# Optimization experiments

Hardware: AMD Instinct MI355X
Metric: run time of the kernel (lower is better)

## Reference

```python
import jax, jax.numpy as jnp
import numpy as np


def setup_inputs() -> dict:
    key = jax.random.key(0)
    k1, k2, k3, k4 = jax.random.split(key, 4)
    N, M, D = 4096, 4096, 1024
    H = jax.random.normal(k1, (N, D), dtype=jnp.float32)
    K = jax.random.normal(k2, (M, D), dtype=jnp.float32)
    V = jax.random.normal(k3, (M, D), dtype=jnp.float32)
    attn_mask = jax.random.uniform(k4, (N, M), dtype=jnp.float32)
    return {"H": H, "K": K, "V": V, "attn_mask": attn_mask}


def reference(H, K, V, attn_mask):
    # scores: [N, M] = H @ K^T, scaled by sqrt(d)
    d = H.shape[1]
    scores = jnp.matmul(H, K.T) / jnp.sqrt(jnp.asarray(d, dtype=H.dtype))
    # double softmax with elementwise mask multiply in between
    probs = jax.nn.softmax(jax.nn.softmax(scores, axis=1) * attn_mask, axis=1)
    return jnp.matmul(probs, V)
```

## Files before the change

### kernel.cpp

```cpp
#include <hip/hip_runtime.h>
#include <cstdint>

typedef unsigned short u16;
typedef __bf16 bf16x8 __attribute__((ext_vector_type(8)));
typedef float f32x4 __attribute__((ext_vector_type(4)));
typedef unsigned int u32x4 __attribute__((ext_vector_type(4)));

__device__ __forceinline__ float bf2f(u16 h) {
  union { unsigned int u; float f; } v; v.u = ((unsigned int)h) << 16; return v.f;
}
__device__ __forceinline__ u16 f2bf(float f) {
  union { float f; unsigned int u; } v; v.f = f;
  unsigned int u = v.u;
  return (u16)((u + 0x7FFFu + ((u >> 16) & 1u)) >> 16);
}

__device__ __forceinline__ void ld_lds16(const void* g, void* l) {
  __builtin_amdgcn_global_load_lds(
      (const __attribute__((address_space(1))) unsigned int*)g,
      (__attribute__((address_space(3))) unsigned int*)l, 16, 0, 0);
}

__global__ __launch_bounds__(512, 2) void gemm1_kernel(
    const u16* __restrict__ A, const u16* __restrict__ B,
    u16* __restrict__ S, int ldA, int ldB, int ldC)
{
  __shared__ __align__(16) u16 smem[65536];

  const int tid  = threadIdx.x;
  const int lane = tid & 63;
  const int w    = tid >> 6;
  const int wr   = w >> 2;
  const int wc   = w & 3;
  const int quad = lane >> 4;
  const int cIn  = lane & 15;
  const int lrow   = lane >> 3;
  const int gchunk = (lane & 7) ^ lrow;

  const int flat = blockIdx.x;
  const int xcd  = flat & 7;
  const int i    = flat >> 3;
  const int rowT = (xcd >> 1) * 4 + (i & 3);
  const int colT = (xcd & 1) * 8 + (i >> 2);
  const int rowBlk = rowT * 256;
  const int colBlk = colT * 256;

  f32x4 acc[8][4];
  #pragma unroll
  for (int a = 0; a < 8; ++a)
    #pragma unroll
    for (int b = 0; b < 4; ++b) acc[a][b] = {0.f, 0.f, 0.f, 0.f};

  auto stageA = [&](int buf, int kt2) {
    #pragma unroll
    for (int l = 0; l < 4; ++l) {
      const u16* ga = A + (size_t)(rowBlk + l * 64 + w * 8 + lrow) * ldA
                        + kt2 * 64 + gchunk * 8;
      ld_lds16(ga, &smem[buf * 16384 + l * 4096 + w * 512]);
    }
  };
  auto stageB = [&](int buf, int kt2) {
    #pragma unroll
    for (int l = 0; l < 4; ++l) {
      const u16* gb = B + (size_t)(colBlk + l * 64 + w * 8 + lrow) * ldB
                        + kt2 * 64 + gchunk * 8;
      ld_lds16(gb, &smem[32768 + buf * 16384 + l * 4096 + w * 512]);
    }
  };

  stageA(0, 0);
  stageB(0, 0);
  stageA(1, 1);
  stageB(1, 1);

  for (int kt = 0; kt < 16; ++kt) {
    const int cur = kt & 1;
    const int aBase = cur * 16384;
    const int bBase = 32768 + cur * 16384;

    if (kt < 15) asm volatile("s_waitcnt vmcnt(8)" ::: "memory");
    else         asm volatile("s_waitcnt vmcnt(0)" ::: "memory");
    __builtin_amdgcn_s_barrier();
    __builtin_amdgcn_sched_barrier(0);

    bf16x8 bf[4][2];
    #pragma unroll
    for (int ni = 0; ni < 4; ++ni)
      #pragma unroll
      for (int ks = 0; ks < 2; ++ks) {
        int row = wc * 64 + ni * 16 + cIn;
        int ch  = (ks * 4 + quad) ^ (row & 7);
        bf[ni][ks] = *(const bf16x8*)&smem[bBase + row * 64 + ch * 8];
      }
    bf16x8 afA[2][2], afB[2][2];
    #pragma unroll
    for (int m = 0; m < 2; ++m)
      #pragma unroll
      for (int ks = 0; ks < 2; ++ks) {
        int row = wr * 128 + m * 16 + cIn;
        int ch  = (ks * 4 + quad) ^ (row & 7);
        afA[m][ks] = *(const bf16x8*)&smem[aBase + row * 64 + ch * 8];
      }

    #pragma unroll
    for (int q = 0; q < 4; ++q) {
      if (q < 3) {
        #pragma unroll
        for (int m = 0; m < 2; ++m)
          #pragma unroll
          for (int ks = 0; ks < 2; ++ks) {
            int row = wr * 128 + ((q + 1) * 2 + m) * 16 + cIn;
            int ch  = (ks * 4 + quad) ^ (row & 7);
            bf16x8 v = *(const bf16x8*)&smem[aBase + row * 64 + ch * 8];
            if (q & 1) afA[m][ks] = v; else afB[m][ks] = v;
          }
      }
      __builtin_amdgcn_sched_barrier(0);
      __builtin_amdgcn_s_barrier();
      __builtin_amdgcn_sched_barrier(0);
      __builtin_amdgcn_s_setprio(1);
      #pragma unroll
      for (int m = 0; m < 2; ++m)
        #pragma unroll
        for (int ni = 0; ni < 4; ++ni)
          #pragma unroll
          for (int ks = 0; ks < 2; ++ks) {
            if (q & 1)
              acc[q * 2 + m][ni] = __builtin_amdgcn_mfma_f32_16x16x32_bf16(
                  afB[m][ks], bf[ni][ks], acc[q * 2 + m][ni], 0, 0, 0);
            else
              acc[q * 2 + m][ni] = __builtin_amdgcn_mfma_f32_16x16x32_bf16(
                  afA[m][ks], bf[ni][ks], acc[q * 2 + m][ni], 0, 0, 0);
          }
      __builtin_amdgcn_s_setprio(0);
      __builtin_amdgcn_sched_barrier(0);
    }
    __builtin_amdgcn_s_barrier();

    if (kt + 2 < 16) {
      stageA(cur, kt + 2);
      stageB(cur, kt + 2);
    }
  }

  const float scale = 0.03125f;
  u16* epi = smem;
  #pragma unroll
  for (int R = 0; R < 2; ++R) {
    #pragma unroll
    for (int m2 = 0; m2 < 4; ++m2) {
      int mi = R * 4 + m2;
      #pragma unroll
      for (int ni = 0; ni < 4; ++ni) {
        int col = wc * 64 + ni * 16 + cIn;
        #pragma unroll
        for (int r = 0; r < 4; ++r) {
          int er = wr * 64 + m2 * 16 + quad * 4 + r;
          epi[er * 264 + col] = f2bf(acc[mi][ni][r] * scale);
        }
      }
    }
    __syncthreads();
    #pragma unroll
    for (int it = 0; it < 8; ++it) {
      int idx = it * 512 + tid;
      int er  = idx >> 5;
      int c8  = idx & 31;
      int grow = rowBlk + (er >> 6) * 128 + R * 64 + (er & 63);
      u32x4 v = *(const u32x4*)&epi[er * 264 + c8 * 8];
      *(u32x4*)&S[(size_t)grow * ldC + colBlk + c8 * 8] = v;
    }
    __syncthreads();
  }
}

__global__ __launch_bounds__(512, 2) void gemm2_kernel(
    const u16* __restrict__ A, const u16* __restrict__ B,
    float* __restrict__ Out, const float* __restrict__ L2,
    int ldA, int ldB, int ldC)
{
  __shared__ __align__(16) u16 smem[49152];

  const int tid  = threadIdx.x;
  const int lane = tid & 63;
  const int w    = tid >> 6;
  const int wk   = w & 1;
  const int wrow = (w >> 1) & 1;
  const int wcol = (w >> 2) & 1;
  const int quad = lane >> 4;
  const int cIn  = lane & 15;
  const int lrow   = lane >> 3;
  const int gchunk = (lane & 7) ^ lrow;

  const int flat = blockIdx.x;
  const int xcd  = flat & 7;
  const int i    = flat >> 3;
  const int rowBlk = (xcd * 4 + (i & 3)) * 128;
  const int colBlk = (i >> 2) * 128;

  f32x4 acc[4][4];
  #pragma unroll
  for (int a = 0; a < 4; ++a)
    #pragma unroll
    for (int b = 0; b < 4; ++b) acc[a][b] = {0.f, 0.f, 0.f, 0.f};

  auto stage = [&](int buf, int kt) {
    int kk = kt * 64;
    #pragma unroll
    for (int t = 0; t < 2; ++t) {
      int rg = w * 2 + t;
      const u16* ga = A + (size_t)(rowBlk + rg * 8 + lrow) * ldA + kk + gchunk * 8;
      ld_lds16(ga, &smem[buf * 8192 + rg * 512]);
      const u16* gb = B + (size_t)(colBlk + rg * 8 + lrow) * ldB + kk + gchunk * 8;
      ld_lds16(gb, &smem[24576 + buf * 8192 + rg * 512]);
    }
  };

  stage(0, 0);
  stage(1, 1);

  int cur = 0;
  for (int kt = 0; kt < 64; ++kt) {
    if (kt < 63) asm volatile("s_waitcnt vmcnt(4)" ::: "memory");
    else         asm volatile("s_waitcnt vmcnt(0)" ::: "memory");
    __builtin_amdgcn_s_barrier();
    __builtin_amdgcn_sched_barrier(0);

    if (kt + 2 < 64) {
      int nb = cur + 2; if (nb >= 3) nb -= 3;
      stage(nb, kt + 2);
    }

    const int aBase = cur * 8192;
    const int bBase = 24576 + cur * 8192;
    bf16x8 af[4], bfr[4];
    #pragma unroll
    for (int mi = 0; mi < 4; ++mi) {
      int row = wrow * 64 + mi * 16 + cIn;
      int ch  = (wk * 4 + quad) ^ (row & 7);
      af[mi]  = *(const bf16x8*)&smem[aBase + row * 64 + ch * 8];
    }
    #pragma unroll
    for (int ni = 0; ni < 4; ++ni) {
      int row = wcol * 64 + ni * 16 + cIn;
      int ch  = (wk * 4 + quad) ^ (row & 7);
      bfr[ni] = *(const bf16x8*)&smem[bBase + row * 64 + ch * 8];
    }
    __builtin_amdgcn_s_setprio(1);
    #pragma unroll
    for (int mi = 0; mi < 4; ++mi)
      #pragma unroll
      for (int ni = 0; ni < 4; ++ni)
        acc[mi][ni] = __builtin_amdgcn_mfma_f32_16x16x32_bf16(
            af[mi], bfr[ni], acc[mi][ni], 0, 0, 0);
    __builtin_amdgcn_s_setprio(0);

    cur = (cur + 1 == 3) ? 0 : cur + 1;
  }

  float* red = (float*)smem;
  const int ow = w >> 1;
  const int rbase = ow * 4160 + lane * 65;
  __syncthreads();
  if (wk == 1) {
    #pragma unroll
    for (int mi = 0; mi < 4; ++mi)
      #pragma unroll
      for (int ni = 0; ni < 4; ++ni)
        #pragma unroll
        for (int r = 0; r < 4; ++r)
          red[rbase + (mi * 4 + ni) * 4 + r] = acc[mi][ni][r];
  }
  __syncthreads();
  if (wk == 0) {
    #pragma unroll
    for (int mi = 0; mi < 4; ++mi) {
      #pragma unroll
      for (int r = 0; r < 4; ++r) {
        int row   = rowBlk + wrow * 64 + mi * 16 + quad * 4 + r;
        float inv = 1.0f / L2[row];
        #pragma unroll
        for (int ni = 0; ni < 4; ++ni) {
          int col = colBlk + wcol * 64 + ni * 16 + cIn;
          float v = acc[mi][ni][r] + red[rbase + (mi * 4 + ni) * 4 + r];
          __builtin_nontemporal_store(v * inv, &Out[(size_t)row * ldC + col]);
        }
      }
    }
  }
}

__global__ __launch_bounds__(256) void prep_kernel(
    const float* __restrict__ H, const float* __restrict__ Kin,
    const float* __restrict__ V, u16* __restrict__ Hb, u16* __restrict__ Kb,
    u16* __restrict__ Vt)
{
  int b = blockIdx.x;
  if (b < 8192) {
    const float* src = (b < 4096) ? H : Kin;
    u16* dst = (b < 4096) ? Hb : Kb;
    int i = (b & 4095) * 256 + threadIdx.x;
    f32x4 v = __builtin_nontemporal_load(&((const f32x4*)src)[i]);
    ushort4 o;
    o.x = f2bf(v.x); o.y = f2bf(v.y); o.z = f2bf(v.z); o.w = f2bf(v.w);
    ((ushort4*)dst)[i] = o;
  } else {
    __shared__ float tile[32][33];
    b -= 8192;
    int c0 = (b & 31) * 32;
    int r0 = (b >> 5) * 32;
    int tx = threadIdx.x & 31, ty = threadIdx.x >> 5;
    #pragma unroll
    for (int s = 0; s < 32; s += 8)
      tile[ty + s][tx] = __builtin_nontemporal_load(
          &V[(size_t)(r0 + ty + s) * 1024 + c0 + tx]);
    __syncthreads();
    if (threadIdx.x < 128) {
      int vr = threadIdx.x >> 2;
      int ch = threadIdx.x & 3;
      u32x4 ov;
      #pragma unroll
      for (int p = 0; p < 4; ++p) {
        unsigned int lo = f2bf(tile[ch * 8 + p * 2][vr]);
        unsigned int hi = f2bf(tile[ch * 8 + p * 2 + 1][vr]);
        ov[p] = lo | (hi << 16);
      }
      *(u32x4*)&Vt[(size_t)(c0 + vr) * 4096 + r0 + ch * 8] = ov;
    }
  }
}

__global__ __launch_bounds__(256) void softmax2_kernel(
    u16* __restrict__ S, const float* __restrict__ mask,
    float* __restrict__ L2, int M)
{
  int row = blockIdx.x;
  u16* srow = S + (size_t)row * M;
  const float* mrow = mask + (size_t)row * M;
  const int base = threadIdx.x * 16;

  u16 sl[16];
  *(uint4*)(sl)     = *(const uint4*)(srow + base);
  *(uint4*)(sl + 8) = *(const uint4*)(srow + base + 8);

  float e[16];
  float s1 = 0.f;
  #pragma unroll
  for (int j = 0; j < 16; ++j) { e[j] = __expf(bf2f(sl[j])); s1 += e[j]; }

  __shared__ float wred[8];
  #pragma unroll
  for (int m = 1; m < 64; m <<= 1) s1 += __shfl_xor(s1, m, 64);
  if ((threadIdx.x & 63) == 0) wred[threadIdx.x >> 6] = s1;
  __syncthreads();
  float inv = 1.0f / (wred[0] + wred[1] + wred[2] + wred[3]);

  float mv[16];
  #pragma unroll
  for (int q = 0; q < 4; ++q) {
    f32x4 m4 = __builtin_nontemporal_load((const f32x4*)(mrow + base + q * 4));
    mv[q * 4 + 0] = m4.x; mv[q * 4 + 1] = m4.y;
    mv[q * 4 + 2] = m4.z; mv[q * 4 + 3] = m4.w;
  }

  float lsum = 0.f;
  #pragma unroll
  for (int j = 0; j < 16; ++j) {
    float p = __expf(e[j] * inv * mv[j]);
    lsum += p;
    sl[j] = f2bf(p);
  }
  *(uint4*)(srow + base)     = *(uint4*)(sl);
  *(uint4*)(srow + base + 8) = *(uint4*)(sl + 8);

  #pragma unroll
  for (int m = 1; m < 64; m <<= 1) lsum += __shfl_xor(lsum, m, 64);
  if ((threadIdx.x & 63) == 0) wred[4 + (threadIdx.x >> 6)] = lsum;
  __syncthreads();
  if (threadIdx.x == 0) L2[row] = wred[4] + wred[5] + wred[6] + wred[7];
}

extern "C" void kernel_launch(void* const* d_in, const int* in_sizes, int n_in,
                              void* d_out, int out_size, void* d_ws, size_t ws_size,
                              hipStream_t stream) {
  const float* H    = (const float*)d_in[0];
  const float* Kin  = (const float*)d_in[1];
  const float* V    = (const float*)d_in[2];
  const float* mask = (const float*)d_in[3];
  float* out = (float*)d_out;

  const int N = 4096, M = 4096, D = 1024;

  char* ws = (char*)d_ws;
  u16*   Hb = (u16*)(ws);
  u16*   Kb = (u16*)(ws + (8ull << 20));
  u16*   Vt = (u16*)(ws + (16ull << 20));
  u16*   S  = (u16*)(ws + (24ull << 20));
  float* L2 = (float*)(ws + (56ull << 20));

  prep_kernel<<<dim3(12288), dim3(256), 0, stream>>>(H, Kin, V, Hb, Kb, Vt);

  gemm1_kernel<<<dim3(256), dim3(512), 0, stream>>>(Hb, Kb, S, D, D, M);

  softmax2_kernel<<<dim3(N), dim3(256), 0, stream>>>(S, mask, L2, M);

  gemm2_kernel<<<dim3(256), dim3(512), 0, stream>>>(S, Vt, out, L2, M, M, D);
}
```

Before: 228.1 us.

## Interleave A-tile global-to-LDS loads per quarter across MFMA phases in gemm1

Splits the A-tile staging into four quarter-sized loads and issues them between the four MFMA phases of each k-step, instead of issuing all A and B loads after the whole k-step finishes. The goal is to spread global-to-LDS traffic through the compute loop, overlap memory latency with MFMA work, and remove the trailing barrier before prefetch. In exchange it adds more barriers and finer vmcnt/lgkmcnt waits whose counts must exactly match outstanding loads, so a miscount could create a race or extra stalls.

```diff
diff --git a/kernel.cpp b/kernel.cpp
--- a/kernel.cpp
+++ b/kernel.cpp
@@ -51,14 +51,6 @@
     #pragma unroll
     for (int b = 0; b < 4; ++b) acc[a][b] = {0.f, 0.f, 0.f, 0.f};
 
-  auto stageA = [&](int buf, int kt2) {
-    #pragma unroll
-    for (int l = 0; l < 4; ++l) {
-      const u16* ga = A + (size_t)(rowBlk + l * 64 + w * 8 + lrow) * ldA
-                        + kt2 * 64 + gchunk * 8;
-      ld_lds16(ga, &smem[buf * 16384 + l * 4096 + w * 512]);
-    }
-  };
   auto stageB = [&](int buf, int kt2) {
     #pragma unroll
     for (int l = 0; l < 4; ++l) {
@@ -67,56 +59,48 @@
       ld_lds16(gb, &smem[32768 + buf * 16384 + l * 4096 + w * 512]);
     }
   };
-
-  stageA(0, 0);
+  auto stageAq = [&](int buf, int kt2, int q) {
+    int rbase = ((w & 4) << 5) + q * 32 + (w & 3) * 8;
+    const u16* ga = A + (size_t)(rowBlk + rbase + lrow) * ldA
+                      + kt2 * 64 + gchunk * 8;
+    ld_lds16(ga, &smem[buf * 16384 + rbase * 64]);
+  };
+
   stageB(0, 0);
-  stageA(1, 1);
+  stageAq(0, 0, 0); stageAq(0, 0, 1); stageAq(0, 0, 2); stageAq(0, 0, 3);
   stageB(1, 1);
+  stageAq(1, 1, 0); stageAq(1, 1, 1); stageAq(1, 1, 2);
+  asm volatile("s_waitcnt vmcnt(10)" ::: "memory");
+  __builtin_amdgcn_s_barrier();
 
   for (int kt = 0; kt < 16; ++kt) {
-    const int cur = kt & 1;
-    const int aBase = cur * 16384;
-    const int bBase = 32768 + cur * 16384;
-
-    if (kt < 15) asm volatile("s_waitcnt vmcnt(8)" ::: "memory");
-    else         asm volatile("s_waitcnt vmcnt(0)" ::: "memory");
-    __builtin_amdgcn_s_barrier();
-    __builtin_amdgcn_sched_barrier(0);
+    const int c = kt & 1;
+    const int aBase = c * 16384;
+    const int bBase = 32768 + c * 16384;
 
     bf16x8 bf[4][2];
-    #pragma unroll
-    for (int ni = 0; ni < 4; ++ni)
-      #pragma unroll
-      for (int ks = 0; ks < 2; ++ks) {
-        int row = wc * 64 + ni * 16 + cIn;
-        int ch  = (ks * 4 + quad) ^ (row & 7);
-        bf[ni][ks] = *(const bf16x8*)&smem[bBase + row * 64 + ch * 8];
-      }
-    bf16x8 afA[2][2], afB[2][2];
-    #pragma unroll
-    for (int m = 0; m < 2; ++m)
-      #pragma unroll
-      for (int ks = 0; ks < 2; ++ks) {
-        int row = wr * 128 + m * 16 + cIn;
-        int ch  = (ks * 4 + quad) ^ (row & 7);
-        afA[m][ks] = *(const bf16x8*)&smem[aBase + row * 64 + ch * 8];
-      }
-
-    #pragma unroll
-    for (int q = 0; q < 4; ++q) {
-      if (q < 3) {
-        #pragma unroll
-        for (int m = 0; m < 2; ++m)
-          #pragma unroll
-          for (int ks = 0; ks < 2; ++ks) {
-            int row = wr * 128 + ((q + 1) * 2 + m) * 16 + cIn;
-            int ch  = (ks * 4 + quad) ^ (row & 7);
-            bf16x8 v = *(const bf16x8*)&smem[aBase + row * 64 + ch * 8];
-            if (q & 1) afA[m][ks] = v; else afB[m][ks] = v;
-          }
-      }
-      __builtin_amdgcn_sched_barrier(0);
+
+    {
+      #pragma unroll
+      for (int ni = 0; ni < 4; ++ni)
+        #pragma unroll
+        for (int ks = 0; ks < 2; ++ks) {
+          int row = wc * 64 + ni * 16 + cIn;
+          int ch  = (ks * 4 + quad) ^ (row & 7);
+          bf[ni][ks] = *(const bf16x8*)&smem[bBase + row * 64 + ch * 8];
+        }
+      bf16x8 af[2][2];
+      #pragma unroll
+      for (int m = 0; m < 2; ++m)
+        #pragma unroll
+        for (int ks = 0; ks < 2; ++ks) {
+          int row = wr * 128 + m * 16 + cIn;
+          int ch  = (ks * 4 + quad) ^ (row & 7);
+          af[m][ks] = *(const bf16x8*)&smem[aBase + row * 64 + ch * 8];
+        }
+      if (kt + 1 < 16) stageAq(c ^ 1, kt + 1, 3);
       __builtin_amdgcn_s_barrier();
+      asm volatile("s_waitcnt lgkmcnt(0)" ::: "memory");
       __builtin_amdgcn_sched_barrier(0);
       __builtin_amdgcn_s_setprio(1);
       #pragma unroll
@@ -124,22 +108,52 @@
         #pragma unroll
         for (int ni = 0; ni < 4; ++ni)
           #pragma unroll
-          for (int ks = 0; ks < 2; ++ks) {
-            if (q & 1)
-              acc[q * 2 + m][ni] = __builtin_amdgcn_mfma_f32_16x16x32_bf16(
-                  afB[m][ks], bf[ni][ks], acc[q * 2 + m][ni], 0, 0, 0);
-            else
-              acc[q * 2 + m][ni] = __builtin_amdgcn_mfma_f32_16x16x32_bf16(
-                  afA[m][ks], bf[ni][ks], acc[q * 2 + m][ni], 0, 0, 0);
-          }
+          for (int ks = 0; ks < 2; ++ks)
+            acc[m][ni] = __builtin_amdgcn_mfma_f32_16x16x32_bf16(
+                af[m][ks], bf[ni][ks], acc[m][ni], 0, 0, 0);
       __builtin_amdgcn_s_setprio(0);
       __builtin_amdgcn_sched_barrier(0);
-    }
-    __builtin_amdgcn_s_barrier();
-
-    if (kt + 2 < 16) {
-      stageA(cur, kt + 2);
-      stageB(cur, kt + 2);
+      if (kt < 14) asm volatile("s_waitcnt vmcnt(10)" ::: "memory");
+      else         asm volatile("s_waitcnt vmcnt(0)" ::: "memory");
+      __builtin_amdgcn_s_barrier();
+    }
+
+    #pragma unroll
+    for (int p = 1; p < 4; ++p) {
+      bf16x8 af[2][2];
+      #pragma unroll
+      for (int m = 0; m < 2; ++m)
+        #pragma unroll
+        for (int ks = 0; ks < 2; ++ks) {
+          int row = wr * 128 + (p * 2 + m) * 16 + cIn;
+          int ch  = (ks * 4 + quad) ^ (row & 7);
+          af[m][ks] = *(const bf16x8*)&smem[aBase + row * 64 + ch * 8];
+        }
+      if (kt + 2 < 16) {
+        if (p == 1) { stageB(c, kt + 2); stageAq(c, kt + 2, 0); }
+        else stageAq(c, kt + 2, p - 1);
+      }
+      __builtin_amdgcn_s_barrier();
+      asm volatile("s_waitcnt lgkmcnt(0)" ::: "memory");
+      __builtin_amdgcn_sched_barrier(0);
+      __builtin_amdgcn_s_setprio(1);
+      #pragma unroll
+      for (int m = 0; m < 2; ++m)
+        #pragma unroll
+        for (int ni = 0; ni < 4; ++ni)
+          #pragma unroll
+          for (int ks = 0; ks < 2; ++ks)
+            acc[p * 2 + m][ni] = __builtin_amdgcn_mfma_f32_16x16x32_bf16(
+                af[m][ks], bf[ni][ks], acc[p * 2 + m][ni], 0, 0, 0);
+      __builtin_amdgcn_s_setprio(0);
+      __builtin_amdgcn_sched_barrier(0);
+      if (kt < 14) {
+        if (p == 3) asm volatile("s_waitcnt vmcnt(10)" ::: "memory");
+        else        asm volatile("s_waitcnt vmcnt(14)" ::: "memory");
+      } else {
+        asm volatile("s_waitcnt vmcnt(0)" ::: "memory");
+      }
+      __builtin_amdgcn_s_barrier();
     }
   }
 
```

After: 227.4 us. Within noise of the previous version (-0.3%).
